# Performance work log

Hardware: AMD Instinct MI355X
Metric: run time of the kernel (lower is better)

Reference implementation:

```python
import jax, jax.numpy as jnp
import numpy as np

H, C = 8, 32          # heads, per-head channels (h_feats)
NEG_SLOPE = 0.2


def setup_inputs() -> dict:
    key = jax.random.key(0)
    ks = jax.random.split(key, 9)
    N, E, F_IN, F_E = 50000, 800000, 128, 16
    x = jax.random.normal(ks[0], (N, F_IN), jnp.float32)
    edge_index = jax.random.randint(ks[1], (2, E), 0, N, jnp.int64)
    edge_attr = jax.random.normal(ks[2], (E, F_E), jnp.float32)
    s = 1.0 / np.sqrt(F_IN)
    W = jax.random.normal(ks[3], (H * C, F_IN), jnp.float32) * s
    W_edge = jax.random.normal(ks[4], (H * C, F_E), jnp.float32) * (1.0 / np.sqrt(F_E))
    att_src = jax.random.normal(ks[5], (H, C), jnp.float32) * (1.0 / np.sqrt(C))
    att_dst = jax.random.normal(ks[6], (H, C), jnp.float32) * (1.0 / np.sqrt(C))
    att_edge = jax.random.normal(ks[7], (H, C), jnp.float32) * (1.0 / np.sqrt(C))
    bias = jnp.zeros((C,), jnp.float32)
    return {"x": x, "edge_index": edge_index, "edge_attr": edge_attr,
            "W": W, "W_edge": W_edge, "att_src": att_src, "att_dst": att_dst,
            "att_edge": att_edge, "bias": bias}


def reference(x, edge_index, edge_attr, W, W_edge, att_src, att_dst, att_edge, bias):
    N = x.shape[0]
    src, dst = edge_index[0], edge_index[1]

    # --- add self loops, edge_attr fill_value='mean' (per-dst mean of incoming attrs) ---
    deg = jax.ops.segment_sum(jnp.ones_like(dst, dtype=edge_attr.dtype), dst, num_segments=N)
    loop_attr = jax.ops.segment_sum(edge_attr, dst, num_segments=N) / jnp.maximum(deg, 1.0)[:, None]
    loop = jnp.arange(N, dtype=src.dtype)
    src = jnp.concatenate([src, loop])
    dst = jnp.concatenate([dst, loop])
    ea = jnp.concatenate([edge_attr, loop_attr], axis=0)  # [E+N, F_e]

    # --- node projection and per-node attention terms ---
    xh = (x @ W.T).reshape(N, H, C)                      # [N,H,C]
    a_src = jnp.einsum('nhc,hc->nh', xh, att_src)        # [N,H]
    a_dst = jnp.einsum('nhc,hc->nh', xh, att_dst)        # [N,H]

    # edge attention folded: (lin_edge(e).view(E,H,C) * att_edge).sum(-1) == e @ M
    M = jnp.einsum('hcf,hc->fh', W_edge.reshape(H, C, -1), att_edge)  # [F_e,H]
    a_edge = ea @ M                                      # [E+N,H]

    alpha = a_src[src] + a_dst[dst] + a_edge             # [E+N,H]
    alpha = jnp.where(alpha >= 0, alpha, NEG_SLOPE * alpha)

    # --- scatter-softmax over edges grouped by dst node ---
    amax = jax.ops.segment_max(alpha, dst, num_segments=N)  # every node has a self loop
    ex = jnp.exp(alpha - amax[dst])
    denom = jax.ops.segment_sum(ex, dst, num_segments=N)
    att = ex / denom[dst]                                # [E+N,H]

    # --- weighted message scatter-sum ---
    msg = xh[src] * att[..., None]                       # [E+N,H,C]
    out = jax.ops.segment_sum(msg, dst, num_segments=N)  # [N,H,C]
    return out.mean(axis=1) + bias                       # concat=False -> head mean
```

## Files before the change

kernel.cpp:

```cpp
#include <hip/hip_runtime.h>
#include <hip/hip_fp16.h>
#include <math.h>

#define H 8
#define C 32
#define HC 256
#define FE 16
#define FIN 128
#define NEG_SLOPE 0.2f

typedef __attribute__((ext_vector_type(8))) short bf16x8;
typedef __attribute__((ext_vector_type(4))) float f32x4;
typedef __attribute__((ext_vector_type(2))) float f32x2;

__device__ __forceinline__ unsigned short f2bf(float f) {
  unsigned int u = __float_as_uint(f);
  unsigned int lsb = (u >> 16) & 1u;
  u += 0x7fffu + lsb;
  return (unsigned short)(u >> 16);
}
__device__ __forceinline__ float bf2f(unsigned short s) {
  return __uint_as_float(((unsigned int)s) << 16);
}
__device__ __forceinline__ unsigned short f2h(float f) {
  return __half_as_ushort(__float2half(f));
}
__device__ __forceinline__ float h2f(unsigned short s) {
  return __half2float(__ushort_as_half(s));
}
__device__ __forceinline__ void pkfma(f32x2& acc, f32x2 x, f32x2 w) {
  asm volatile("v_pk_fma_f32 %0, %1, %2, %0" : "+v"(acc) : "v"(x), "v"(w));
}

__device__ __forceinline__ void split8(const float* v, bf16x8& hi, bf16x8& lo) {
#pragma unroll
  for (int i = 0; i < 8; ++i) {
    unsigned int u = __float_as_uint(v[i]);
    unsigned int hu = u & 0xffff0000u;
    float r = v[i] - __uint_as_float(hu);
    hi[i] = (short)(hu >> 16);
    lo[i] = (short)f2bf(r);
  }
}

__global__ __launch_bounds__(256) void k_fused(const float* __restrict__ x,
                                               const float* __restrict__ W,
                                               const float* __restrict__ att_src,
                                               const float* __restrict__ att_dst,
                                               const int* __restrict__ ei,
                                               int* __restrict__ deg,
                                               int* __restrict__ rank,
                                               unsigned short* __restrict__ xhb,
                                               float* __restrict__ a_dst,
                                               unsigned short* __restrict__ a_srch,
                                               int N, int E, int nx) {
  int t = threadIdx.x;
  if ((int)blockIdx.x >= 2 * nx) {
    int ebase = (blockIdx.x - 2 * nx) * 2048 + t;
    int dv[8];
#pragma unroll
    for (int k = 0; k < 8; ++k) {
      int e = ebase + k * 256;
      dv[k] = (e < E) ? ei[E + e] : -1;
    }
    int rv[8];
#pragma unroll
    for (int k = 0; k < 8; ++k)
      if (dv[k] >= 0) rv[k] = atomicAdd(&deg[dv[k]], 1);
#pragma unroll
    for (int k = 0; k < 8; ++k) {
      int e = ebase + k * 256;
      if (e < E) rank[e] = rv[k];
    }
    return;
  }
  int bb = blockIdx.x;
  int by = (bb >= nx) ? 1 : 0;
  int bx = bb - by * nx;

  int w = t >> 6, lane = t & 63;
  int n15 = lane & 15, q = lane >> 4;
  int nodeBase = bx * 128 + w * 32;
  int chBase = by * 128;

  f32x4 acc[8][2];
#pragma unroll
  for (int mt = 0; mt < 8; ++mt)
#pragma unroll
    for (int nt = 0; nt < 2; ++nt) acc[mt][nt] = (f32x4)(0.f);

  for (int ks = 0; ks < 4; ++ks) {
    int kOff = ks * 32 + q * 8;
    bf16x8 Bhi[2], Blo[2];
#pragma unroll
    for (int nt = 0; nt < 2; ++nt) {
      int node = nodeBase + nt * 16 + n15;
      int rn = (node < N) ? node : (N - 1);
      const float* px = &x[(size_t)rn * FIN + kOff];
      float vb[8];
      *(float4*)&vb[0] = *(const float4*)px;
      *(float4*)&vb[4] = *(const float4*)(px + 4);
      split8(vb, Bhi[nt], Blo[nt]);
    }
#pragma unroll
    for (int mt = 0; mt < 8; ++mt) {
      int widx = ((chBase + mt * 16 + n15) << 7) + kOff;
      const float* pw = &W[widx];
      float wv8[8];
      *(float4*)&wv8[0] = *(const float4*)pw;
      *(float4*)&wv8[4] = *(const float4*)(pw + 4);
      bf16x8 Ahi, Alo;
      split8(wv8, Ahi, Alo);
#pragma unroll
      for (int nt = 0; nt < 2; ++nt) {
        acc[mt][nt] = __builtin_amdgcn_mfma_f32_16x16x32_bf16(Ahi, Bhi[nt], acc[mt][nt], 0, 0, 0);
        acc[mt][nt] = __builtin_amdgcn_mfma_f32_16x16x32_bf16(Ahi, Blo[nt], acc[mt][nt], 0, 0, 0);
        acc[mt][nt] = __builtin_amdgcn_mfma_f32_16x16x32_bf16(Alo, Bhi[nt], acc[mt][nt], 0, 0, 0);
      }
    }
  }

  float ps[2][4] = {{0.f,0.f,0.f,0.f},{0.f,0.f,0.f,0.f}};
  float pd[2][4] = {{0.f,0.f,0.f,0.f},{0.f,0.f,0.f,0.f}};
#pragma unroll
  for (int mt = 0; mt < 8; ++mt) {
    int hl = mt >> 1;
#pragma unroll
    for (int r = 0; r < 4; ++r) {
      int ch = chBase + mt * 16 + q * 4 + r;
      float as_c = att_src[ch], ad_c = att_dst[ch];
#pragma unroll
      for (int nt = 0; nt < 2; ++nt) {
        float val = acc[mt][nt][r];
        ps[nt][hl] = fmaf(val, as_c, ps[nt][hl]);
        pd[nt][hl] = fmaf(val, ad_c, pd[nt][hl]);
      }
    }
#pragma unroll
    for (int nt = 0; nt < 2; ++nt) {
      int node = nodeBase + nt * 16 + n15;
      if (node < N) {
        ushort4 us;
        us.x = f2bf(acc[mt][nt][0]); us.y = f2bf(acc[mt][nt][1]);
        us.z = f2bf(acc[mt][nt][2]); us.w = f2bf(acc[mt][nt][3]);
        *(ushort4*)&xhb[(size_t)node * HC + chBase + mt * 16 + q * 4] = us;
      }
    }
  }
#pragma unroll
  for (int nt = 0; nt < 2; ++nt)
#pragma unroll
    for (int hl = 0; hl < 4; ++hl) {
      ps[nt][hl] += __shfl_xor(ps[nt][hl], 16, 64);
      ps[nt][hl] += __shfl_xor(ps[nt][hl], 32, 64);
      pd[nt][hl] += __shfl_xor(pd[nt][hl], 16, 64);
      pd[nt][hl] += __shfl_xor(pd[nt][hl], 32, 64);
    }
  if (q == 0) {
#pragma unroll
    for (int nt = 0; nt < 2; ++nt) {
      int node = nodeBase + nt * 16 + n15;
      if (node < N) {
        *(float4*)&a_dst[node * H + by * 4] = make_float4(pd[nt][0], pd[nt][1], pd[nt][2], pd[nt][3]);
        unsigned int p0 = (unsigned int)f2h(ps[nt][0]) | ((unsigned int)f2h(ps[nt][1]) << 16);
        unsigned int p1 = (unsigned int)f2h(ps[nt][2]) | ((unsigned int)f2h(ps[nt][3]) << 16);
        *(uint2*)&a_srch[(size_t)node * H + by * 4] = make_uint2(p0, p1);
      }
    }
  }
}

__global__ __launch_bounds__(256) void k_scan(const int* __restrict__ deg,
                                              int* __restrict__ rowptr, int N, int E) {
  __shared__ int csum[256];
  __shared__ int buf[256];
  int t = threadIdx.x;
  int nb = (N + 255) >> 8;
  int s = 0;
  if (t < nb) {
    int base = t << 8;
    int end = base + 256; if (end > N) end = N;
    for (int i = base; i < end; ++i) s += deg[i];
  }
  csum[t] = s;
  __syncthreads();
  for (int off = 1; off < 256; off <<= 1) {
    int y = (t >= off) ? csum[t - off] : 0;
    __syncthreads();
    csum[t] += y;
    __syncthreads();
  }
  int bofs = (blockIdx.x == 0) ? 0 : csum[blockIdx.x - 1];
  int i = blockIdx.x * 256 + t;
  int v = (i < N) ? deg[i] : 0;
  buf[t] = v;
  __syncthreads();
  for (int off = 1; off < 256; off <<= 1) {
    int y = (t >= off) ? buf[t - off] : 0;
    __syncthreads();
    buf[t] += y;
    __syncthreads();
  }
  if (i < N) rowptr[i] = bofs + buf[t] - v;
  if (i == 0) rowptr[N] = E;
}

__global__ __launch_bounds__(256) void k_edge_scatter(const int* __restrict__ ei,
                                                      const float* __restrict__ ea,
                                                      const float* __restrict__ W_edge,
                                                      const float* __restrict__ att_edge,
                                                      const unsigned short* __restrict__ a_srch,
                                                      const int* __restrict__ rowptr,
                                                      const int* __restrict__ rank,
                                                      unsigned int* __restrict__ recs,
                                                      int* __restrict__ sarr, int E) {
  __shared__ float Ms[FE * H];
  int t = threadIdx.x;
  if (t < FE * H) {
    int f = t >> 3, h = t & 7;
    float acc = 0.f;
#pragma unroll
    for (int c = 0; c < C; ++c)
      acc += W_edge[(h * C + c) * FE + f] * att_edge[h * C + c];
    Ms[f * H + h] = acc;
  }
  __syncthreads();
  int e0 = blockIdx.x * 512 + t;
  int e1 = e0 + 256;
  bool va = (e0 < E), vb = (e1 < E);
  int ca = va ? e0 : 0, cb = vb ? e1 : 0;
  int s0 = ei[ca], d0 = ei[E + ca];
  int s1 = ei[cb], d1 = ei[E + cb];
  const float4* pA = (const float4*)&ea[(size_t)ca * FE];
  const float4* pB = (const float4*)&ea[(size_t)cb * FE];
  float4 A0 = pA[0], A1 = pA[1], A2 = pA[2], A3 = pA[3];
  float4 B0 = pB[0], B1 = pB[1], B2 = pB[2], B3 = pB[3];
  int rk0 = rank[ca], rk1 = rank[cb];
  int rp0 = rowptr[d0], rp1 = rowptr[d1];
  uint4 asA = *(const uint4*)&a_srch[(size_t)s0 * H];
  uint4 asB = *(const uint4*)&a_srch[(size_t)s1 * H];

  float eavA[FE] = {A0.x, A0.y, A0.z, A0.w, A1.x, A1.y, A1.z, A1.w,
                    A2.x, A2.y, A2.z, A2.w, A3.x, A3.y, A3.z, A3.w};
  float eavB[FE] = {B0.x, B0.y, B0.z, B0.w, B1.x, B1.y, B1.z, B1.w,
                    B2.x, B2.y, B2.z, B2.w, B3.x, B3.y, B3.z, B3.w};
  float oA[H], oB[H];
#pragma unroll
  for (int h = 0; h < H; ++h) {
    float aa = 0.f, ab = 0.f;
#pragma unroll
    for (int f = 0; f < FE; ++f) {
      float m = Ms[f * H + h];
      aa += eavA[f] * m;
      ab += eavB[f] * m;
    }
    oA[h] = aa; oB[h] = ab;
  }
  unsigned int asw[2][4] = {{asA.x, asA.y, asA.z, asA.w}, {asB.x, asB.y, asB.z, asB.w}};
  if (va) {
    int pos = rp0 + rk0;
    unsigned int rec[H];
#pragma unroll
    for (int h = 0; h < H; ++h) {
      float asv = h2f((unsigned short)((h & 1) ? (asw[0][h >> 1] >> 16) : (asw[0][h >> 1] & 0xffffu)));
      rec[h] = (unsigned int)f2h(oA[h] + asv) | ((unsigned int)f2h(oA[h]) << 16);
    }
    uint4* rp = (uint4*)&recs[(size_t)pos * 8];
    rp[0] = make_uint4(rec[0], rec[1], rec[2], rec[3]);
    rp[1] = make_uint4(rec[4], rec[5], rec[6], rec[7]);
    sarr[pos] = s0;
  }
  if (vb) {
    int pos = rp1 + rk1;
    unsigned int rec[H];
#pragma unroll
    for (int h = 0; h < H; ++h) {
      float asv = h2f((unsigned short)((h & 1) ? (asw[1][h >> 1] >> 16) : (asw[1][h >> 1] & 0xffffu)));
      rec[h] = (unsigned int)f2h(oB[h] + asv) | ((unsigned int)f2h(oB[h]) << 16);
    }
    uint4* rp = (uint4*)&recs[(size_t)pos * 8];
    rp[0] = make_uint4(rec[0], rec[1], rec[2], rec[3]);
    rp[1] = make_uint4(rec[4], rec[5], rec[6], rec[7]);
    sarr[pos] = s1;
  }
}

__global__ __launch_bounds__(256) void k_node(const unsigned short* __restrict__ xhb,
                                              const unsigned short* __restrict__ a_srch,
                                              const float* __restrict__ a_dst,
                                              const unsigned int* __restrict__ recs,
                                              const int* __restrict__ sarr,
                                              const int* __restrict__ rowptr,
                                              const float* __restrict__ bias,
                                              float* __restrict__ out, int N) {
  __shared__ float wlds[4][512];
  __shared__ int   slds[4][64];
  int wv = threadIdx.x >> 6;
  int lane = threadIdx.x & 63;
  int n = blockIdx.x * 4 + wv;
  if (n >= N) return;
  int start = rowptr[n];
  int deg = rowptr[n + 1] - start;
  int jmax = (deg < 64) ? deg : 64;
  int nit = (jmax + 7) >> 3;
  int padded = nit << 3;
  int h = lane & 7, esub = lane >> 3;
  float adst = a_dst[n * H + h];
  float asrc = h2f(a_srch[(size_t)n * H + h]);

  if (lane < padded) slds[wv][lane] = (lane < jmax) ? sarr[start + lane] : n;

  const unsigned int* rb = recs + (size_t)start * 8 + lane;
  unsigned int u[8] = {0, 0, 0, 0, 0, 0, 0, 0};
#pragma unroll
  for (int it = 0; it < 8; ++it)
    if (it < nit) {
      int j = it * 8 + esub;
      if (j < jmax) u[it] = rb[it * 64];
    }

  int widx = ((esub >> 1) << 4) + (h << 1) + (esub & 1);
  float den = 0.f, psum = 0.f;
#pragma unroll
  for (int it = 0; it < 8; ++it)
    if (it < nit) {
      int j = it * 8 + esub;
      bool val = (j < jmax);
      float raw = h2f((unsigned short)(u[it] >> 16));
      float a = h2f((unsigned short)(u[it] & 0xffffu)) + adst;
      a = fmaxf(a, NEG_SLOPE * a);
      float w = val ? __expf(a) : 0.f;
      psum += val ? raw : 0.f;
      den += w;
      wlds[wv][it * 64 + widx] = w;
    }
  for (int j0 = 64; j0 < deg; j0 += 8) {
    int j = j0 + esub;
    if (j < deg) {
      unsigned int t2 = recs[(size_t)(start + j) * 8 + h];
      psum += h2f((unsigned short)(t2 >> 16));
      float a = h2f((unsigned short)(t2 & 0xffffu)) + adst;
      a = fmaxf(a, NEG_SLOPE * a);
      den += __expf(a);
    }
  }
#pragma unroll
  for (int m = 8; m <= 32; m <<= 1) {
    den += __shfl_xor(den, m, 64);
    psum += __shfl_xor(psum, m, 64);
  }
  float aself = asrc + adst + psum / fmaxf((float)deg, 1.f);
  aself = fmaxf(aself, NEG_SLOPE * aself);
  float wself = __expf(aself);
  float inv = 1.f / (den + wself);

  int hc = lane >> 3;
  float inv_c  = __shfl(inv, hc, 64);
  float ws_c   = __shfl(wself, hc, 64);
  float adst_c = __shfl(adst, hc, 64);
  f32x2 A0, A1, A2, A3;
  {
    uint2 su = ((const uint2*)(xhb + (((size_t)n) << 8)))[lane];
    A0[0] = ws_c * __uint_as_float(su.x << 16);         A0[1] = 0.f;
    A1[0] = ws_c * __uint_as_float(su.x & 0xffff0000u); A1[1] = 0.f;
    A2[0] = ws_c * __uint_as_float(su.y << 16);         A2[1] = 0.f;
    A3[0] = ws_c * __uint_as_float(su.y & 0xffff0000u); A3[1] = 0.f;
  }
  for (int j0 = 0; j0 < padded; j0 += 8) {
    uint2 v[8];
#pragma unroll
    for (int k = 0; k < 8; ++k)
      v[k] = ((const uint2*)(xhb + (((size_t)slds[wv][j0 + k]) << 8)))[lane];
#pragma unroll
    for (int k2 = 0; k2 < 4; ++k2) {
      f32x2 wp = *(const f32x2*)&wlds[wv][j0 * 8 + k2 * 16 + hc * 2];
      uint2 va = v[2 * k2], vb2 = v[2 * k2 + 1];
      f32x2 p;
      p[0] = __uint_as_float(va.x << 16);          p[1] = __uint_as_float(vb2.x << 16);
      pkfma(A0, p, wp);
      p[0] = __uint_as_float(va.x & 0xffff0000u);  p[1] = __uint_as_float(vb2.x & 0xffff0000u);
      pkfma(A1, p, wp);
      p[0] = __uint_as_float(va.y << 16);          p[1] = __uint_as_float(vb2.y << 16);
      pkfma(A2, p, wp);
      p[0] = __uint_as_float(va.y & 0xffff0000u);  p[1] = __uint_as_float(vb2.y & 0xffff0000u);
      pkfma(A3, p, wp);
    }
  }
  float accx = A0[0] + A0[1];
  float accy = A1[0] + A1[1];
  float accz = A2[0] + A2[1];
  float accw = A3[0] + A3[1];
  for (int j = 64; j < deg; ++j) {
    int src = sarr[start + j];
    unsigned int t2 = recs[(size_t)(start + j) * 8 + hc];
    float a = h2f((unsigned short)(t2 & 0xffffu)) + adst_c;
    a = fmaxf(a, NEG_SLOPE * a);
    float wj = __expf(a);
    uint2 v = ((const uint2*)(xhb + (((size_t)src) << 8)))[lane];
    accx = fmaf(__uint_as_float(v.x << 16), wj, accx);
    accy = fmaf(__uint_as_float(v.x & 0xffff0000u), wj, accy);
    accz = fmaf(__uint_as_float(v.y << 16), wj, accz);
    accw = fmaf(__uint_as_float(v.y & 0xffff0000u), wj, accw);
  }
  accx *= inv_c; accy *= inv_c; accz *= inv_c; accw *= inv_c;

#pragma unroll
  for (int m = 8; m <= 32; m <<= 1) {
    accx += __shfl_xor(accx, m, 64);
    accy += __shfl_xor(accy, m, 64);
    accz += __shfl_xor(accz, m, 64);
    accw += __shfl_xor(accw, m, 64);
  }
  if (lane < 8) {
    float4 b = ((const float4*)bias)[lane];
    float4 o;
    o.x = accx * 0.125f + b.x;
    o.y = accy * 0.125f + b.y;
    o.z = accz * 0.125f + b.z;
    o.w = accw * 0.125f + b.w;
    ((float4*)&out[(size_t)n * C])[lane] = o;
  }
}

extern "C" void kernel_launch(void* const* d_in, const int* in_sizes, int n_in,
                              void* d_out, int out_size, void* d_ws, size_t ws_size,
                              hipStream_t stream) {
  const float* x        = (const float*)d_in[0];
  const int*   ei       = (const int*)d_in[1];
  const float* ea       = (const float*)d_in[2];
  const float* W        = (const float*)d_in[3];
  const float* W_edge   = (const float*)d_in[4];
  const float* att_src  = (const float*)d_in[5];
  const float* att_dst  = (const float*)d_in[6];
  const float* att_edge = (const float*)d_in[7];
  const float* bias     = (const float*)d_in[8];
  float* out = (float*)d_out;

  int N = in_sizes[0] / FIN;
  int E = in_sizes[1] / 2;
  int nb = (N + 255) / 256;
  int nh = (E + 2047) / 2048;
  int nx = (N + 127) / 128;

  char* ws = (char*)d_ws;
  auto take = [&](size_t bytes) {
    char* p = ws;
    ws += (bytes + 255) & ~(size_t)255;
    return p;
  };
  unsigned short* xhb    = (unsigned short*)take((size_t)N * HC * 2);
  float*          a_dst  = (float*)take((size_t)N * H * 4);
  unsigned short* a_srch = (unsigned short*)take((size_t)N * H * 2);
  unsigned int*   recs   = (unsigned int*)take((size_t)E * 32);
  int*            sarr   = (int*)take((size_t)E * 4);
  int*            deg    = (int*)take((size_t)N * 4);
  int*            rowptr = (int*)take((size_t)(N + 1) * 4);
  int*            rank   = (int*)take((size_t)E * 4);

  hipMemsetAsync(deg, 0, (size_t)N * 4, stream);
  k_fused<<<nh + 2 * nx, 256, 0, stream>>>(x, W, att_src, att_dst, ei, deg, rank,
                                           xhb, a_dst, a_srch, N, E, nx);
  k_scan<<<nb, 256, 0, stream>>>(deg, rowptr, N, E);
  k_edge_scatter<<<(E + 511) / 512, 256, 0, stream>>>(ei, ea, W_edge, att_edge, a_srch, rowptr, rank, recs, sarr, E);
  k_node<<<(N + 3) / 4, 256, 0, stream>>>(xhb, a_srch, a_dst, recs, sarr, rowptr, bias, out, N);
}
```

Before: 301.2 us.

## Merge projection, degree count, scan and edge scatter into one persistent kernel

Replaces three separate kernels (the fused GEMM plus degree-count kernel, the scan, and the edge scatter) with one persistent kernel that uses grid-stride loops and two software grid barriers built on an atomic counter. The goal is to remove kernel launch gaps and tail effects between the stages. In exchange it adds spin-wait barriers and relies on every block being co-resident, which it tries to ensure by sizing the grid from the occupancy query. The memset now also clears the barrier counter, and the degree count moves to one edge per thread.

Result: slower. 1.091 ms (+262.3%).

```diff
diff --git a/kernel.cpp b/kernel.cpp
--- a/kernel.cpp
+++ b/kernel.cpp
@@ -43,179 +43,180 @@
   }
 }
 
-__global__ __launch_bounds__(256) void k_fused(const float* __restrict__ x,
-                                               const float* __restrict__ W,
-                                               const float* __restrict__ att_src,
-                                               const float* __restrict__ att_dst,
-                                               const int* __restrict__ ei,
-                                               int* __restrict__ deg,
-                                               int* __restrict__ rank,
-                                               unsigned short* __restrict__ xhb,
-                                               float* __restrict__ a_dst,
-                                               unsigned short* __restrict__ a_srch,
-                                               int N, int E, int nx) {
-  int t = threadIdx.x;
-  if ((int)blockIdx.x >= 2 * nx) {
-    int ebase = (blockIdx.x - 2 * nx) * 2048 + t;
-    int dv[8];
-#pragma unroll
-    for (int k = 0; k < 8; ++k) {
-      int e = ebase + k * 256;
-      dv[k] = (e < E) ? ei[E + e] : -1;
-    }
-    int rv[8];
-#pragma unroll
-    for (int k = 0; k < 8; ++k)
-      if (dv[k] >= 0) rv[k] = atomicAdd(&deg[dv[k]], 1);
-#pragma unroll
-    for (int k = 0; k < 8; ++k) {
-      int e = ebase + k * 256;
-      if (e < E) rank[e] = rv[k];
-    }
-    return;
-  }
-  int bb = blockIdx.x;
-  int by = (bb >= nx) ? 1 : 0;
-  int bx = bb - by * nx;
-
-  int w = t >> 6, lane = t & 63;
-  int n15 = lane & 15, q = lane >> 4;
-  int nodeBase = bx * 128 + w * 32;
-  int chBase = by * 128;
-
-  f32x4 acc[8][2];
-#pragma unroll
-  for (int mt = 0; mt < 8; ++mt)
-#pragma unroll
-    for (int nt = 0; nt < 2; ++nt) acc[mt][nt] = (f32x4)(0.f);
-
-  for (int ks = 0; ks < 4; ++ks) {
-    int kOff = ks * 32 + q * 8;
-    bf16x8 Bhi[2], Blo[2];
-#pragma unroll
-    for (int nt = 0; nt < 2; ++nt) {
-      int node = nodeBase + nt * 16 + n15;
-      int rn = (node < N) ? node : (N - 1);
-      const float* px = &x[(size_t)rn * FIN + kOff];
-      float vb[8];
-      *(float4*)&vb[0] = *(const float4*)px;
-      *(float4*)&vb[4] = *(const float4*)(px + 4);
-      split8(vb, Bhi[nt], Blo[nt]);
-    }
-#pragma unroll
-    for (int mt = 0; mt < 8; ++mt) {
-      int widx = ((chBase + mt * 16 + n15) << 7) + kOff;
-      const float* pw = &W[widx];
-      float wv8[8];
-      *(float4*)&wv8[0] = *(const float4*)pw;
-      *(float4*)&wv8[4] = *(const float4*)(pw + 4);
-      bf16x8 Ahi, Alo;
-      split8(wv8, Ahi, Alo);
-#pragma unroll
-      for (int nt = 0; nt < 2; ++nt) {
-        acc[mt][nt] = __builtin_amdgcn_mfma_f32_16x16x32_bf16(Ahi, Bhi[nt], acc[mt][nt], 0, 0, 0);
-        acc[mt][nt] = __builtin_amdgcn_mfma_f32_16x16x32_bf16(Ahi, Blo[nt], acc[mt][nt], 0, 0, 0);
-        acc[mt][nt] = __builtin_amdgcn_mfma_f32_16x16x32_bf16(Alo, Bhi[nt], acc[mt][nt], 0, 0, 0);
-      }
-    }
-  }
-
-  float ps[2][4] = {{0.f,0.f,0.f,0.f},{0.f,0.f,0.f,0.f}};
-  float pd[2][4] = {{0.f,0.f,0.f,0.f},{0.f,0.f,0.f,0.f}};
-#pragma unroll
-  for (int mt = 0; mt < 8; ++mt) {
-    int hl = mt >> 1;
-#pragma unroll
-    for (int r = 0; r < 4; ++r) {
-      int ch = chBase + mt * 16 + q * 4 + r;
-      float as_c = att_src[ch], ad_c = att_dst[ch];
-#pragma unroll
-      for (int nt = 0; nt < 2; ++nt) {
-        float val = acc[mt][nt][r];
-        ps[nt][hl] = fmaf(val, as_c, ps[nt][hl]);
-        pd[nt][hl] = fmaf(val, ad_c, pd[nt][hl]);
-      }
-    }
-#pragma unroll
-    for (int nt = 0; nt < 2; ++nt) {
-      int node = nodeBase + nt * 16 + n15;
-      if (node < N) {
-        ushort4 us;
-        us.x = f2bf(acc[mt][nt][0]); us.y = f2bf(acc[mt][nt][1]);
-        us.z = f2bf(acc[mt][nt][2]); us.w = f2bf(acc[mt][nt][3]);
-        *(ushort4*)&xhb[(size_t)node * HC + chBase + mt * 16 + q * 4] = us;
-      }
-    }
-  }
-#pragma unroll
-  for (int nt = 0; nt < 2; ++nt)
-#pragma unroll
-    for (int hl = 0; hl < 4; ++hl) {
-      ps[nt][hl] += __shfl_xor(ps[nt][hl], 16, 64);
-      ps[nt][hl] += __shfl_xor(ps[nt][hl], 32, 64);
-      pd[nt][hl] += __shfl_xor(pd[nt][hl], 16, 64);
-      pd[nt][hl] += __shfl_xor(pd[nt][hl], 32, 64);
-    }
-  if (q == 0) {
-#pragma unroll
-    for (int nt = 0; nt < 2; ++nt) {
-      int node = nodeBase + nt * 16 + n15;
-      if (node < N) {
-        *(float4*)&a_dst[node * H + by * 4] = make_float4(pd[nt][0], pd[nt][1], pd[nt][2], pd[nt][3]);
-        unsigned int p0 = (unsigned int)f2h(ps[nt][0]) | ((unsigned int)f2h(ps[nt][1]) << 16);
-        unsigned int p1 = (unsigned int)f2h(ps[nt][2]) | ((unsigned int)f2h(ps[nt][3]) << 16);
-        *(uint2*)&a_srch[(size_t)node * H + by * 4] = make_uint2(p0, p1);
-      }
-    }
-  }
-}
-
-__global__ __launch_bounds__(256) void k_scan(const int* __restrict__ deg,
-                                              int* __restrict__ rowptr, int N, int E) {
+__device__ __forceinline__ void gbar(int* cnt, int target) {
+  __threadfence();
+  __syncthreads();
+  if (threadIdx.x == 0) {
+    __hip_atomic_fetch_add(cnt, 1, __ATOMIC_ACQ_REL, __HIP_MEMORY_SCOPE_AGENT);
+    while (__hip_atomic_load(cnt, __ATOMIC_ACQUIRE, __HIP_MEMORY_SCOPE_AGENT) < target)
+      __builtin_amdgcn_s_sleep(1);
+  }
+  __syncthreads();
+  __threadfence();
+}
+
+__global__ __launch_bounds__(256, 4) void k_mega(const float* __restrict__ x,
+                                                 const float* __restrict__ W,
+                                                 const float* __restrict__ att_src,
+                                                 const float* __restrict__ att_dst,
+                                                 const int* __restrict__ ei,
+                                                 const float* __restrict__ ea,
+                                                 const float* __restrict__ W_edge,
+                                                 const float* __restrict__ att_edge,
+                                                 int* __restrict__ deg,
+                                                 int* __restrict__ rank,
+                                                 unsigned short* __restrict__ xhb,
+                                                 float* __restrict__ a_dst,
+                                                 unsigned short* __restrict__ a_srch,
+                                                 int* __restrict__ rowptr,
+                                                 unsigned int* __restrict__ recs,
+                                                 int* __restrict__ sarr,
+                                                 int* __restrict__ cnt,
+                                                 int N, int E, int nx) {
   __shared__ int csum[256];
-  __shared__ int buf[256];
-  int t = threadIdx.x;
-  int nb = (N + 255) >> 8;
-  int s = 0;
-  if (t < nb) {
-    int base = t << 8;
-    int end = base + 256; if (end > N) end = N;
-    for (int i = base; i < end; ++i) s += deg[i];
-  }
-  csum[t] = s;
-  __syncthreads();
-  for (int off = 1; off < 256; off <<= 1) {
-    int y = (t >= off) ? csum[t - off] : 0;
-    __syncthreads();
-    csum[t] += y;
-    __syncthreads();
-  }
-  int bofs = (blockIdx.x == 0) ? 0 : csum[blockIdx.x - 1];
-  int i = blockIdx.x * 256 + t;
-  int v = (i < N) ? deg[i] : 0;
-  buf[t] = v;
-  __syncthreads();
-  for (int off = 1; off < 256; off <<= 1) {
-    int y = (t >= off) ? buf[t - off] : 0;
-    __syncthreads();
-    buf[t] += y;
-    __syncthreads();
-  }
-  if (i < N) rowptr[i] = bofs + buf[t] - v;
-  if (i == 0) rowptr[N] = E;
-}
-
-__global__ __launch_bounds__(256) void k_edge_scatter(const int* __restrict__ ei,
-                                                      const float* __restrict__ ea,
-                                                      const float* __restrict__ W_edge,
-                                                      const float* __restrict__ att_edge,
-                                                      const unsigned short* __restrict__ a_srch,
-                                                      const int* __restrict__ rowptr,
-                                                      const int* __restrict__ rank,
-                                                      unsigned int* __restrict__ recs,
-                                                      int* __restrict__ sarr, int E) {
+  __shared__ int sbuf[256];
   __shared__ float Ms[FE * H];
   int t = threadIdx.x;
+  int NB = gridDim.x;
+
+  int nGemm = 2 * nx;
+  for (int vb = blockIdx.x; vb < nGemm; vb += NB) {
+    int by = (vb >= nx) ? 1 : 0;
+    int bx = vb - by * nx;
+    int w = t >> 6, lane = t & 63;
+    int n15 = lane & 15, q = lane >> 4;
+    int nodeBase = bx * 128 + w * 32;
+    int chBase = by * 128;
+
+    f32x4 acc[8][2];
+#pragma unroll
+    for (int mt = 0; mt < 8; ++mt)
+#pragma unroll
+      for (int nt = 0; nt < 2; ++nt) acc[mt][nt] = (f32x4)(0.f);
+
+    for (int ks = 0; ks < 4; ++ks) {
+      int kOff = ks * 32 + q * 8;
+      bf16x8 Bhi[2], Blo[2];
+#pragma unroll
+      for (int nt = 0; nt < 2; ++nt) {
+        int node = nodeBase + nt * 16 + n15;
+        int rn = (node < N) ? node : (N - 1);
+        const float* px = &x[(size_t)rn * FIN + kOff];
+        float vbuf[8];
+        *(float4*)&vbuf[0] = *(const float4*)px;
+        *(float4*)&vbuf[4] = *(const float4*)(px + 4);
+        split8(vbuf, Bhi[nt], Blo[nt]);
+      }
+#pragma unroll
+      for (int mt = 0; mt < 8; ++mt) {
+        int widx = ((chBase + mt * 16 + n15) << 7) + kOff;
+        const float* pw = &W[widx];
+        float wv8[8];
+        *(float4*)&wv8[0] = *(const float4*)pw;
+        *(float4*)&wv8[4] = *(const float4*)(pw + 4);
+        bf16x8 Ahi, Alo;
+        split8(wv8, Ahi, Alo);
+#pragma unroll
+        for (int nt = 0; nt < 2; ++nt) {
+          acc[mt][nt] = __builtin_amdgcn_mfma_f32_16x16x32_bf16(Ahi, Bhi[nt], acc[mt][nt], 0, 0, 0);
+          acc[mt][nt] = __builtin_amdgcn_mfma_f32_16x16x32_bf16(Ahi, Blo[nt], acc[mt][nt], 0, 0, 0);
+          acc[mt][nt] = __builtin_amdgcn_mfma_f32_16x16x32_bf16(Alo, Bhi[nt], acc[mt][nt], 0, 0, 0);
+        }
+      }
+    }
+
+    float ps[2][4] = {{0.f,0.f,0.f,0.f},{0.f,0.f,0.f,0.f}};
+    float pd[2][4] = {{0.f,0.f,0.f,0.f},{0.f,0.f,0.f,0.f}};
+#pragma unroll
+    for (int mt = 0; mt < 8; ++mt) {
+      int hl = mt >> 1;
+#pragma unroll
+      for (int r = 0; r < 4; ++r) {
+        int ch = chBase + mt * 16 + q * 4 + r;
+        float as_c = att_src[ch], ad_c = att_dst[ch];
+#pragma unroll
+        for (int nt = 0; nt < 2; ++nt) {
+          float val = acc[mt][nt][r];
+          ps[nt][hl] = fmaf(val, as_c, ps[nt][hl]);
+          pd[nt][hl] = fmaf(val, ad_c, pd[nt][hl]);
+        }
+      }
+#pragma unroll
+      for (int nt = 0; nt < 2; ++nt) {
+        int node = nodeBase + nt * 16 + n15;
+        if (node < N) {
+          ushort4 us;
+          us.x = f2bf(acc[mt][nt][0]); us.y = f2bf(acc[mt][nt][1]);
+          us.z = f2bf(acc[mt][nt][2]); us.w = f2bf(acc[mt][nt][3]);
+          *(ushort4*)&xhb[(size_t)node * HC + chBase + mt * 16 + q * 4] = us;
+        }
+      }
+    }
+#pragma unroll
+    for (int nt = 0; nt < 2; ++nt)
+#pragma unroll
+      for (int hl = 0; hl < 4; ++hl) {
+        ps[nt][hl] += __shfl_xor(ps[nt][hl], 16, 64);
+        ps[nt][hl] += __shfl_xor(ps[nt][hl], 32, 64);
+        pd[nt][hl] += __shfl_xor(pd[nt][hl], 16, 64);
+        pd[nt][hl] += __shfl_xor(pd[nt][hl], 32, 64);
+      }
+    if (q == 0) {
+#pragma unroll
+      for (int nt = 0; nt < 2; ++nt) {
+        int node = nodeBase + nt * 16 + n15;
+        if (node < N) {
+          *(float4*)&a_dst[node * H + by * 4] = make_float4(pd[nt][0], pd[nt][1], pd[nt][2], pd[nt][3]);
+          unsigned int p0 = (unsigned int)f2h(ps[nt][0]) | ((unsigned int)f2h(ps[nt][1]) << 16);
+          unsigned int p1 = (unsigned int)f2h(ps[nt][2]) | ((unsigned int)f2h(ps[nt][3]) << 16);
+          *(uint2*)&a_srch[(size_t)node * H + by * 4] = make_uint2(p0, p1);
+        }
+      }
+    }
+  }
+
+  int nhc = (E + 255) >> 8;
+  for (int vc = blockIdx.x; vc < nhc; vc += NB) {
+    int e = (vc << 8) + t;
+    if (e < E) rank[e] = atomicAdd(&deg[ei[E + e]], 1);
+  }
+
+  gbar(cnt, NB);
+
+  int nbs = (N + 255) >> 8;
+  for (int vb = blockIdx.x; vb < nbs; vb += NB) {
+    int s = 0;
+    if (t < nbs) {
+      int base = t << 8;
+      int end = base + 256; if (end > N) end = N;
+      for (int i = base; i < end; ++i) s += deg[i];
+    }
+    csum[t] = s;
+    __syncthreads();
+    for (int off = 1; off < 256; off <<= 1) {
+      int y = (t >= off) ? csum[t - off] : 0;
+      __syncthreads();
+      csum[t] += y;
+      __syncthreads();
+    }
+    int bofs = (vb == 0) ? 0 : csum[vb - 1];
+    int i = vb * 256 + t;
+    int v = (i < N) ? deg[i] : 0;
+    sbuf[t] = v;
+    __syncthreads();
+    for (int off = 1; off < 256; off <<= 1) {
+      int y = (t >= off) ? sbuf[t - off] : 0;
+      __syncthreads();
+      sbuf[t] += y;
+      __syncthreads();
+    }
+    if (i < N) rowptr[i] = bofs + sbuf[t] - v;
+    if (i == 0) rowptr[N] = E;
+    __syncthreads();
+  }
+
+  gbar(cnt, 2 * NB);
+
   if (t < FE * H) {
     int f = t >> 3, h = t & 7;
     float acc = 0.f;
@@ -225,63 +226,67 @@
     Ms[f * H + h] = acc;
   }
   __syncthreads();
-  int e0 = blockIdx.x * 512 + t;
-  int e1 = e0 + 256;
-  bool va = (e0 < E), vb = (e1 < E);
-  int ca = va ? e0 : 0, cb = vb ? e1 : 0;
-  int s0 = ei[ca], d0 = ei[E + ca];
-  int s1 = ei[cb], d1 = ei[E + cb];
-  const float4* pA = (const float4*)&ea[(size_t)ca * FE];
-  const float4* pB = (const float4*)&ea[(size_t)cb * FE];
-  float4 A0 = pA[0], A1 = pA[1], A2 = pA[2], A3 = pA[3];
-  float4 B0 = pB[0], B1 = pB[1], B2 = pB[2], B3 = pB[3];
-  int rk0 = rank[ca], rk1 = rank[cb];
-  int rp0 = rowptr[d0], rp1 = rowptr[d1];
-  uint4 asA = *(const uint4*)&a_srch[(size_t)s0 * H];
-  uint4 asB = *(const uint4*)&a_srch[(size_t)s1 * H];
-
-  float eavA[FE] = {A0.x, A0.y, A0.z, A0.w, A1.x, A1.y, A1.z, A1.w,
-                    A2.x, A2.y, A2.z, A2.w, A3.x, A3.y, A3.z, A3.w};
-  float eavB[FE] = {B0.x, B0.y, B0.z, B0.w, B1.x, B1.y, B1.z, B1.w,
-                    B2.x, B2.y, B2.z, B2.w, B3.x, B3.y, B3.z, B3.w};
-  float oA[H], oB[H];
-#pragma unroll
-  for (int h = 0; h < H; ++h) {
-    float aa = 0.f, ab = 0.f;
-#pragma unroll
-    for (int f = 0; f < FE; ++f) {
-      float m = Ms[f * H + h];
-      aa += eavA[f] * m;
-      ab += eavB[f] * m;
-    }
-    oA[h] = aa; oB[h] = ab;
-  }
-  unsigned int asw[2][4] = {{asA.x, asA.y, asA.z, asA.w}, {asB.x, asB.y, asB.z, asB.w}};
-  if (va) {
-    int pos = rp0 + rk0;
-    unsigned int rec[H];
+
+  int nec = (E + 511) >> 9;
+  for (int vb = blockIdx.x; vb < nec; vb += NB) {
+    int e0 = vb * 512 + t;
+    int e1 = e0 + 256;
+    bool va = (e0 < E), vbv = (e1 < E);
+    int ca = va ? e0 : 0, cb = vbv ? e1 : 0;
+    int s0 = ei[ca], d0 = ei[E + ca];
+    int s1 = ei[cb], d1 = ei[E + cb];
+    const float4* pA = (const float4*)&ea[(size_t)ca * FE];
+    const float4* pB = (const float4*)&ea[(size_t)cb * FE];
+    float4 A0 = pA[0], A1 = pA[1], A2 = pA[2], A3 = pA[3];
+    float4 B0 = pB[0], B1 = pB[1], B2 = pB[2], B3 = pB[3];
+    int rk0 = rank[ca], rk1 = rank[cb];
+    int rp0 = rowptr[d0], rp1 = rowptr[d1];
+    uint4 asA = *(const uint4*)&a_srch[(size_t)s0 * H];
+    uint4 asB = *(const uint4*)&a_srch[(size_t)s1 * H];
+
+    float eavA[FE] = {A0.x, A0.y, A0.z, A0.w, A1.x, A1.y, A1.z, A1.w,
+                      A2.x, A2.y, A2.z, A2.w, A3.x, A3.y, A3.z, A3.w};
+    float eavB[FE] = {B0.x, B0.y, B0.z, B0.w, B1.x, B1.y, B1.z, B1.w,
+                      B2.x, B2.y, B2.z, B2.w, B3.x, B3.y, B3.z, B3.w};
+    float oA[H], oB[H];
 #pragma unroll
     for (int h = 0; h < H; ++h) {
-      float asv = h2f((unsigned short)((h & 1) ? (asw[0][h >> 1] >> 16) : (asw[0][h >> 1] & 0xffffu)));
-      rec[h] = (unsigned int)f2h(oA[h] + asv) | ((unsigned int)f2h(oA[h]) << 16);
-    }
-    uint4* rp = (uint4*)&recs[(size_t)pos * 8];
-    rp[0] = make_uint4(rec[0], rec[1], rec[2], rec[3]);
-    rp[1] = make_uint4(rec[4], rec[5], rec[6], rec[7]);
-    sarr[pos] = s0;
-  }
-  if (vb) {
-    int pos = rp1 + rk1;
-    unsigned int rec[H];
-#pragma unroll
-    for (int h = 0; h < H; ++h) {
-      float asv = h2f((unsigned short)((h & 1) ? (asw[1][h >> 1] >> 16) : (asw[1][h >> 1] & 0xffffu)));
-      rec[h] = (unsigned int)f2h(oB[h] + asv) | ((unsigned int)f2h(oB[h]) << 16);
-    }
-    uint4* rp = (uint4*)&recs[(size_t)pos * 8];
-    rp[0] = make_uint4(rec[0], rec[1], rec[2], rec[3]);
-    rp[1] = make_uint4(rec[4], rec[5], rec[6], rec[7]);
-    sarr[pos] = s1;
+      float aa = 0.f, ab = 0.f;
+#pragma unroll
+      for (int f = 0; f < FE; ++f) {
+        float m = Ms[f * H + h];
+        aa += eavA[f] * m;
+        ab += eavB[f] * m;
+      }
+      oA[h] = aa; oB[h] = ab;
+    }
+    unsigned int asw[2][4] = {{asA.x, asA.y, asA.z, asA.w}, {asB.x, asB.y, asB.z, asB.w}};
+    if (va) {
+      int pos = rp0 + rk0;
+      unsigned int rec[H];
+#pragma unroll
+      for (int h = 0; h < H; ++h) {
+        float asv = h2f((unsigned short)((h & 1) ? (asw[0][h >> 1] >> 16) : (asw[0][h >> 1] & 0xffffu)));
+        rec[h] = (unsigned int)f2h(oA[h] + asv) | ((unsigned int)f2h(oA[h]) << 16);
+      }
+      uint4* rp = (uint4*)&recs[(size_t)pos * 8];
+      rp[0] = make_uint4(rec[0], rec[1], rec[2], rec[3]);
+      rp[1] = make_uint4(rec[4], rec[5], rec[6], rec[7]);
+      sarr[pos] = s0;
+    }
+    if (vbv) {
+      int pos = rp1 + rk1;
+      unsigned int rec[H];
+#pragma unroll
+      for (int h = 0; h < H; ++h) {
+        float asv = h2f((unsigned short)((h & 1) ? (asw[1][h >> 1] >> 16) : (asw[1][h >> 1] & 0xffffu)));
+        rec[h] = (unsigned int)f2h(oB[h] + asv) | ((unsigned int)f2h(oB[h]) << 16);
+      }
+      uint4* rp = (uint4*)&recs[(size_t)pos * 8];
+      rp[0] = make_uint4(rec[0], rec[1], rec[2], rec[3]);
+      rp[1] = make_uint4(rec[4], rec[5], rec[6], rec[7]);
+      sarr[pos] = s1;
+    }
   }
 }
 
@@ -438,8 +443,6 @@
 
   int N = in_sizes[0] / FIN;
   int E = in_sizes[1] / 2;
-  int nb = (N + 255) / 256;
-  int nh = (E + 2047) / 2048;
   int nx = (N + 127) / 128;
 
   char* ws = (char*)d_ws;
@@ -453,14 +456,21 @@
   unsigned short* a_srch = (unsigned short*)take((size_t)N * H * 2);
   unsigned int*   recs   = (unsigned int*)take((size_t)E * 32);
   int*            sarr   = (int*)take((size_t)E * 4);
-  int*            deg    = (int*)take((size_t)N * 4);
   int*            rowptr = (int*)take((size_t)(N + 1) * 4);
   int*            rank   = (int*)take((size_t)E * 4);
-
-  hipMemsetAsync(deg, 0, (size_t)N * 4, stream);
-  k_fused<<<nh + 2 * nx, 256, 0, stream>>>(x, W, att_src, att_dst, ei, deg, rank,
-                                           xhb, a_dst, a_srch, N, E, nx);
-  k_scan<<<nb, 256, 0, stream>>>(deg, rowptr, N, E);
-  k_edge_scatter<<<(E + 511) / 512, 256, 0, stream>>>(ei, ea, W_edge, att_edge, a_srch, rowptr, rank, recs, sarr, E);
+  char*           zbase  = take((size_t)N * 4 + 256);
+  int*            deg    = (int*)zbase;
+  int*            cnt    = (int*)(zbase + (size_t)N * 4);
+
+  int occ = 4;
+  (void)hipOccupancyMaxActiveBlocksPerMultiprocessor(&occ, k_mega, 256, 0);
+  if (occ < 1) occ = 1;
+  int NB = occ * 256;
+  if (NB > 1024) NB = 1024;
+
+  hipMemsetAsync(zbase, 0, (size_t)N * 4 + 256, stream);
+  k_mega<<<NB, 256, 0, stream>>>(x, W, att_src, att_dst, ei, ea, W_edge, att_edge,
+                                 deg, rank, xhb, a_dst, a_srch, rowptr, recs, sarr, cnt,
+                                 N, E, nx);
   k_node<<<(N + 3) / 4, 256, 0, stream>>>(xhb, a_srch, a_dst, recs, sarr, rowptr, bias, out, N);
 }
```
